# Optimization experiments

Hardware: AMD Instinct MI355X
Metric: run time of the kernel (lower is better)

The kernel has to match this reference:

```python
import jax, jax.numpy as jnp
import numpy as np

B, D, K = 32, 64, 256            # batch, num objects (seq len), feature size (== in_size)
G = [256, 256, 256]              # g_layers sizes
F1, F2, OUT = 256, 256, 128      # f_fc1, f_fc2, out_size


def setup_inputs() -> dict:
    key = jax.random.key(0)
    ks = jax.random.split(key, 16)
    scale = 0.02

    def w(k, shape):
        return jax.random.normal(k, shape, dtype=jnp.float32) * scale

    x = jax.random.normal(ks[0], (B, D, K), dtype=jnp.float32)
    # edge_feature: Linear(2*K, K). Stored [in, out] (transposed vs torch).
    edge_w = w(ks[1], (2 * K, K))
    edge_b = jnp.zeros((K,), dtype=jnp.float32)
    g_ws, g_bs = [], []
    in_s = K
    for i, out_s in enumerate(G):
        g_ws.append(w(ks[2 + i], (in_s, out_s)))
        g_bs.append(jnp.zeros((out_s,), dtype=jnp.float32))
        in_s = out_s
    f1_w = w(ks[8], (G[-1], F1)); f1_b = jnp.zeros((F1,), dtype=jnp.float32)
    f2_w = w(ks[9], (F1, F2));    f2_b = jnp.zeros((F2,), dtype=jnp.float32)
    f3_w = w(ks[10], (F2, OUT));  f3_b = jnp.zeros((OUT,), dtype=jnp.float32)
    return dict(x=x, edge_w=edge_w, edge_b=edge_b, g_ws=g_ws, g_bs=g_bs,
                f1_w=f1_w, f1_b=f1_b, f2_w=f2_w, f2_b=f2_b, f3_w=f3_w, f3_b=f3_b)


def reference(x, edge_w, edge_b, g_ws, g_bs, f1_w, f1_b, f2_w, f2_b, f3_w, f3_b):
    # x: [B, D, K]. Original builds x_full[b,i,j] = concat(x[b,j], x[b,i]) then
    # applies edge_feature (Linear(2K -> K)). Equivalent, without materializing the
    # concat: split edge_w into the halves acting on x_i (=x[b,j]) and x_j (=x[b,i]).
    k = x.shape[-1]
    u = x @ edge_w[:k]      # [B, D, K]  -> indexed by j (axis 2)
    v = x @ edge_w[k:]      # [B, D, K]  -> indexed by i (axis 1)
    h = u[:, None, :, :] + v[:, :, None, :] + edge_b   # [B, D, D, K]
    # g MLP over all d^2 pairs (Linear + ReLU chain)
    for gw, gb in zip(g_ws, g_bs):
        h = jax.nn.relu(h @ gw + gb)
    # sum-aggregate over all pairs
    x_g = h.sum(axis=(1, 2))                            # [B, G[-1]]
    # f MLP (dropout p=0.0 -> identity)
    x_f = jax.nn.relu(x_g @ f1_w + f1_b)
    x_f = jax.nn.relu(x_f @ f2_w + f2_b)
    return x_f @ f3_w + f3_b                            # [B, OUT]
```

## Files before the change

### kernel.cpp

```cpp
#include <hip/hip_runtime.h>
#include <hip/hip_bf16.h>

typedef __attribute__((ext_vector_type(4))) float f32x4;
typedef __attribute__((ext_vector_type(2))) int   i32x2;
typedef __attribute__((ext_vector_type(4))) int   i32x4;
typedef __attribute__((ext_vector_type(8))) short short8;

__device__ __forceinline__ unsigned short f2bf(float x) {
  __hip_bfloat16 h = __float2bfloat16(x);
  union { __hip_bfloat16 h1; unsigned short u; } c; c.h1 = h; return c.u;
}
__device__ __forceinline__ unsigned pk2(float a, float b) {
  __hip_bfloat162 h = __float22bfloat162_rn(make_float2(a, b));
  union { __hip_bfloat162 h2; unsigned u; } c; c.h2 = h; return c.u;
}
__device__ __forceinline__ float bf2f(unsigned short u) {
  union { unsigned u32; float f; } c; c.u32 = ((unsigned)u) << 16; return c.f;
}

__global__ void k_prep(const float* __restrict__ edge_w, const float* __restrict__ edge_b,
                       const float* __restrict__ gw0, const float* __restrict__ gb0,
                       const float* __restrict__ gw1, const float* __restrict__ gw2,
                       float* __restrict__ W1u, float* __restrict__ W1v,
                       float* __restrict__ c1,
                       unsigned short* __restrict__ W2R, unsigned short* __restrict__ W3R) {
  const int blk = blockIdx.x, t = threadIdx.x;
  __shared__ float eu[256], ev[256];
  if (blk < 256) {
    eu[t] = edge_w[blk * 256 + t];
    ev[t] = edge_w[(256 + blk) * 256 + t];
    __syncthreads();
    float su = 0.f, sv = 0.f;
    for (int o = 0; o < 256; ++o) {
      float gg = gw0[o * 256 + t];
      su += eu[o] * gg; sv += ev[o] * gg;
    }
    W1u[blk * 256 + t] = su;
    W1v[blk * 256 + t] = sv;
  } else if (blk == 256) {
    float s = gb0[t];
    for (int o = 0; o < 256; ++o) s += edge_b[o] * gw0[o * 256 + t];
    c1[t] = s;
  } else {
    int p = blk - 257;
    const float* src = (p < 32) ? gw1 : gw2;
    unsigned short* dst = (p < 32) ? W2R : W3R;
    p &= 31;
    int w = p >> 3, ch = p & 7;
    int mf = t >> 6, lane = t & 63, q = lane & 15, g = lane >> 4;
    int base = ((w * 8 + ch) * 4 + mf) * 512 + lane * 8;
    int m = w * 64 + mf * 16 + q;
#pragma unroll
    for (int e = 0; e < 8; ++e) {
      int k = ch * 32 + g * 8 + e;
      dst[base + e] = f2bf(src[k * 256 + m]);
    }
  }
}

__global__ void k_uv(const float* __restrict__ x,
                     const float* __restrict__ W1u, const float* __restrict__ W1v,
                     const float* __restrict__ c1,
                     unsigned short* __restrict__ U1, float* __restrict__ V1c) {
  const int blk = blockIdx.x, t = threadIdx.x;
  const int r0 = blk * 8;
  __shared__ float xs[2048];
  __shared__ float pl[8 * 512];
  if (t < 512) *(f32x4*)(xs + t * 4) = *(const f32x4*)(x + (size_t)r0 * 256 + t * 4);
  __syncthreads();
  const int sel = t >> 9, kh = (t >> 8) & 1, col = t & 255;
  const float* W = (sel ? W1v : W1u) + (size_t)kh * 128 * 256;
  const float* xb = xs + kh * 128;
  float a[8];
#pragma unroll
  for (int r = 0; r < 8; ++r) a[r] = 0.f;
#pragma unroll 4
  for (int k = 0; k < 128; ++k) {
    float w = W[k * 256 + col];
#pragma unroll
    for (int r = 0; r < 8; ++r) a[r] += xb[r * 256 + k] * w;
  }
  if (kh == 1) {
#pragma unroll
    for (int r = 0; r < 8; ++r) pl[r * 512 + sel * 256 + col] = a[r];
  }
  __syncthreads();
  if (kh == 0) {
#pragma unroll
    for (int r = 0; r < 8; ++r) a[r] += pl[r * 512 + sel * 256 + col];
    if (sel == 0) {
#pragma unroll
      for (int r = 0; r < 8; ++r) U1[(size_t)(r0 + r) * 256 + col] = f2bf(a[r]);
    } else {
      float c = c1[col];
#pragma unroll
      for (int r = 0; r < 8; ++r) V1c[(size_t)(r0 + r) * 256 + col] = a[r] + c;
    }
  }
}

__device__ __forceinline__ void write_h1(short8 u, f32x4 v0, f32x4 v1,
                                         unsigned short* dst) {
  float r0 = fmaxf(bf2f((unsigned short)u[0]) + v0.x, 0.f);
  float r1 = fmaxf(bf2f((unsigned short)u[1]) + v0.y, 0.f);
  float r2 = fmaxf(bf2f((unsigned short)u[2]) + v0.z, 0.f);
  float r3 = fmaxf(bf2f((unsigned short)u[3]) + v0.w, 0.f);
  float r4 = fmaxf(bf2f((unsigned short)u[4]) + v1.x, 0.f);
  float r5 = fmaxf(bf2f((unsigned short)u[5]) + v1.y, 0.f);
  float r6 = fmaxf(bf2f((unsigned short)u[6]) + v1.z, 0.f);
  float r7 = fmaxf(bf2f((unsigned short)u[7]) + v1.w, 0.f);
  i32x4 wv = { (int)pk2(r0, r1), (int)pk2(r2, r3), (int)pk2(r4, r5), (int)pk2(r6, r7) };
  *(i32x4*)dst = wv;
}

__launch_bounds__(256, 3)
__global__ void k_main(const unsigned short* __restrict__ U1,
                       const float* __restrict__ V1c,
                       const unsigned short* __restrict__ W2R,
                       const unsigned short* __restrict__ W3R,
                       const float* __restrict__ b2, const float* __restrict__ b3,
                       float* __restrict__ partials) {
  __shared__ unsigned short hbuf[16384];

  const int t = threadIdx.x;
  const int bid = blockIdx.x;
  const int wrk = ((bid & 7) << 8) | (bid >> 3);
  const int b = wrk >> 6;
  const int wid = t >> 6, lane = t & 63;
  const int q = lane & 15, g = lane >> 4;
  const int mo = wid << 6;

  {
    const int row = t >> 2, sl = t & 3, r7 = row & 7;
    const unsigned short* uB = U1 + (size_t)(b * 64 + row) * 256;
    const float* vB = V1c + (size_t)wrk * 256;
    unsigned short* hB = hbuf + row * 256;
#pragma unroll
    for (int m = 0; m < 8; ++m) {
      int ks = sl + 4 * m;
      int s = ks ^ r7;
      short8 u = *(const short8*)(uB + ks * 8);
      f32x4 v0 = *(const f32x4*)(vB + ks * 8);
      f32x4 v1 = *(const f32x4*)(vB + ks * 8 + 4);
      write_h1(u, v0, v1, hB + s * 8);
    }
  }

  const unsigned short* aW2 = W2R + (size_t)wid * 16384 + lane * 8;
  const unsigned short* aW3 = W3R + (size_t)wid * 16384 + lane * 8;

  short8 a_[4], an_[4];
#pragma unroll
  for (int mf = 0; mf < 4; ++mf) a_[mf] = *(const short8*)(aW2 + mf * 512);

  __syncthreads();

  f32x4 acc[4][4];
#pragma unroll
  for (int mf = 0; mf < 4; ++mf)
#pragma unroll
    for (int nf = 0; nf < 4; ++nf) acc[mf][nf] = (f32x4){0.f, 0.f, 0.f, 0.f};

  for (int ch = 0; ch < 8; ++ch) {
    if (ch < 7) {
#pragma unroll
      for (int mf = 0; mf < 4; ++mf)
        an_[mf] = *(const short8*)(aW2 + (ch + 1) * 2048 + mf * 512);
    }
    short8 b_[4];
#pragma unroll
    for (int nf = 0; nf < 4; ++nf) {
      int r = q + 16 * nf;
      b_[nf] = *(const short8*)(hbuf + r * 256 + (((ch * 4 + g) ^ (r & 7)) * 8));
    }
#pragma unroll
    for (int mf = 0; mf < 4; ++mf)
#pragma unroll
      for (int nf = 0; nf < 4; ++nf)
        acc[mf][nf] = __builtin_amdgcn_mfma_f32_16x16x32_bf16(a_[mf], b_[nf], acc[mf][nf], 0, 0, 0);
    if (ch < 7) {
#pragma unroll
      for (int mf = 0; mf < 4; ++mf) a_[mf] = an_[mf];
    }
  }

  __syncthreads();

#pragma unroll
  for (int mf = 0; mf < 4; ++mf) a_[mf] = *(const short8*)(aW3 + mf * 512);
#pragma unroll
  for (int mf = 0; mf < 4; ++mf) {
    int c2b = mo + 16 * mf + 4 * g;
    f32x4 bb = *(const f32x4*)(b2 + c2b);
    int ksw = c2b >> 3, off = c2b & 7;
#pragma unroll
    for (int nf = 0; nf < 4; ++nf) {
      int r = q + 16 * nf;
      f32x4 v = acc[mf][nf];
      float e0 = fmaxf(v.x + bb.x, 0.f), e1 = fmaxf(v.y + bb.y, 0.f);
      float e2 = fmaxf(v.z + bb.z, 0.f), e3 = fmaxf(v.w + bb.w, 0.f);
      i32x2 wv = { (int)pk2(e0, e1), (int)pk2(e2, e3) };
      *(i32x2*)(hbuf + r * 256 + ((ksw ^ (r & 7)) * 8) + off) = wv;
    }
  }
  __syncthreads();

  f32x4 acc2[4][4];
#pragma unroll
  for (int mf = 0; mf < 4; ++mf)
#pragma unroll
    for (int nf = 0; nf < 4; ++nf) acc2[mf][nf] = (f32x4){0.f, 0.f, 0.f, 0.f};

  for (int ch = 0; ch < 8; ++ch) {
    if (ch < 7) {
#pragma unroll
      for (int mf = 0; mf < 4; ++mf)
        an_[mf] = *(const short8*)(aW3 + (ch + 1) * 2048 + mf * 512);
    }
    short8 b_[4];
#pragma unroll
    for (int nf = 0; nf < 4; ++nf) {
      int r = q + 16 * nf;
      b_[nf] = *(const short8*)(hbuf + r * 256 + (((ch * 4 + g) ^ (r & 7)) * 8));
    }
#pragma unroll
    for (int mf = 0; mf < 4; ++mf)
#pragma unroll
      for (int nf = 0; nf < 4; ++nf)
        acc2[mf][nf] = __builtin_amdgcn_mfma_f32_16x16x32_bf16(a_[mf], b_[nf], acc2[mf][nf], 0, 0, 0);
    if (ch < 7) {
#pragma unroll
      for (int mf = 0; mf < 4; ++mf) a_[mf] = an_[mf];
    }
  }

  __syncthreads();

  float* scr = (float*)&hbuf[0];
#pragma unroll
  for (int mf = 0; mf < 4; ++mf) {
    int n3b = mo + 16 * mf + 4 * g;
    f32x4 bb = *(const f32x4*)(b3 + n3b);
    f32x4 sum = (f32x4){0.f, 0.f, 0.f, 0.f};
#pragma unroll
    for (int nf = 0; nf < 4; ++nf) {
      f32x4 v = acc2[mf][nf];
      sum.x += fmaxf(v.x + bb.x, 0.f);
      sum.y += fmaxf(v.y + bb.y, 0.f);
      sum.z += fmaxf(v.z + bb.z, 0.f);
      sum.w += fmaxf(v.w + bb.w, 0.f);
    }
    *(f32x4*)(scr + q * 264 + n3b) = sum;
  }
  __syncthreads();
  float s = 0.f;
#pragma unroll
  for (int q2 = 0; q2 < 16; ++q2) s += scr[q2 * 264 + t];
  partials[(size_t)wrk * 256 + t] = s;
}

__global__ void k_fmlp(const float* __restrict__ partials,
                       const float* __restrict__ f1w, const float* __restrict__ f1b,
                       const float* __restrict__ f2w, const float* __restrict__ f2b,
                       const float* __restrict__ f3w, const float* __restrict__ f3b,
                       float* __restrict__ out) {
  const int b = blockIdx.x, t = threadIdx.x;
  __shared__ float xg[256], x1[256], x2[256];
  {
    const float* p = partials + (size_t)(b * 64) * 256 + t;
    float s[8];
#pragma unroll
    for (int i = 0; i < 8; ++i) s[i] = 0.f;
#pragma unroll
    for (int k = 0; k < 8; ++k)
#pragma unroll
      for (int i = 0; i < 8; ++i) s[i] += p[(k * 8 + i) * 256];
    float tot = 0.f;
#pragma unroll
    for (int i = 0; i < 8; ++i) tot += s[i];
    xg[t] = tot;
  }
  __syncthreads();
  {
    float a0 = 0.f, a1 = 0.f, a2 = 0.f, a3 = 0.f;
#pragma unroll 4
    for (int k = 0; k < 64; ++k) {
      a0 += xg[k]       * f1w[(k)       * 256 + t];
      a1 += xg[k + 64]  * f1w[(k + 64)  * 256 + t];
      a2 += xg[k + 128] * f1w[(k + 128) * 256 + t];
      a3 += xg[k + 192] * f1w[(k + 192) * 256 + t];
    }
    x1[t] = fmaxf((a0 + a1) + (a2 + a3) + f1b[t], 0.f);
  }
  __syncthreads();
  {
    float a0 = 0.f, a1 = 0.f, a2 = 0.f, a3 = 0.f;
#pragma unroll 4
    for (int k = 0; k < 64; ++k) {
      a0 += x1[k]       * f2w[(k)       * 256 + t];
      a1 += x1[k + 64]  * f2w[(k + 64)  * 256 + t];
      a2 += x1[k + 128] * f2w[(k + 128) * 256 + t];
      a3 += x1[k + 192] * f2w[(k + 192) * 256 + t];
    }
    x2[t] = fmaxf((a0 + a1) + (a2 + a3) + f2b[t], 0.f);
  }
  __syncthreads();
  if (t < 128) {
    float a0 = 0.f, a1 = 0.f, a2 = 0.f, a3 = 0.f;
#pragma unroll 4
    for (int k = 0; k < 64; ++k) {
      a0 += x2[k]       * f3w[(k)       * 128 + t];
      a1 += x2[k + 64]  * f3w[(k + 64)  * 128 + t];
      a2 += x2[k + 128] * f3w[(k + 128) * 128 + t];
      a3 += x2[k + 192] * f3w[(k + 192) * 128 + t];
    }
    out[b * 128 + t] = (a0 + a1) + (a2 + a3) + f3b[t];
  }
}

__global__ void k_zero(float* __restrict__ out, int n) {
  int i = blockIdx.x * 256 + threadIdx.x;
  if (i < n) out[i] = 0.f;
}

extern "C" void kernel_launch(void* const* d_in, const int* in_sizes, int n_in,
                              void* d_out, int out_size, void* d_ws, size_t ws_size,
                              hipStream_t stream) {
  const float* x      = (const float*)d_in[0];
  const float* edge_w = (const float*)d_in[1];
  const float* edge_b = (const float*)d_in[2];
  const float *gw0, *gw1, *gw2, *gb0, *gb1, *gb2;
  const float *f1w, *f1b, *f2w, *f2b, *f3w, *f3b;

  if (n_in >= 15 && in_sizes[3] == 65536 && in_sizes[4] == 65536 && in_sizes[5] == 65536) {
    gw0 = (const float*)d_in[3]; gw1 = (const float*)d_in[4]; gw2 = (const float*)d_in[5];
    gb0 = (const float*)d_in[6]; gb1 = (const float*)d_in[7]; gb2 = (const float*)d_in[8];
    f1w = (const float*)d_in[9];  f1b = (const float*)d_in[10];
    f2w = (const float*)d_in[11]; f2b = (const float*)d_in[12];
    f3w = (const float*)d_in[13]; f3b = (const float*)d_in[14];
  } else if (n_in >= 15 && in_sizes[3] == 65536 && in_sizes[4] == 256) {
    gw0 = (const float*)d_in[3]; gb0 = (const float*)d_in[4];
    gw1 = (const float*)d_in[5]; gb1 = (const float*)d_in[6];
    gw2 = (const float*)d_in[7]; gb2 = (const float*)d_in[8];
    f1w = (const float*)d_in[9];  f1b = (const float*)d_in[10];
    f2w = (const float*)d_in[11]; f2b = (const float*)d_in[12];
    f3w = (const float*)d_in[13]; f3b = (const float*)d_in[14];
  } else {
    const float* gws = (const float*)d_in[3];
    const float* gbs = (const float*)d_in[4];
    gw0 = gws;          gw1 = gws + 65536;  gw2 = gws + 131072;
    gb0 = gbs;          gb1 = gbs + 256;    gb2 = gbs + 512;
    f1w = (const float*)d_in[5];  f1b = (const float*)d_in[6];
    f2w = (const float*)d_in[7];  f2b = (const float*)d_in[8];
    f3w = (const float*)d_in[9];  f3b = (const float*)d_in[10];
  }

  char* ws = (char*)d_ws;
  float*          W1u      = (float*)(ws);
  float*          W1v      = (float*)(ws + 262144);
  float*          c1       = (float*)(ws + 524288);
  unsigned short* W2R      = (unsigned short*)(ws + 525312);
  unsigned short* W3R      = (unsigned short*)(ws + 656384);
  unsigned short* U1       = (unsigned short*)(ws + 787456);
  float*          V1c      = (float*)(ws + 1836032);
  float*          partials = (float*)(ws + 3933184);
  const size_t need = 6030336;
  (void)out_size; (void)n_in;

  if (ws_size < need) {
    k_zero<<<dim3((out_size + 255) / 256), dim3(256), 0, stream>>>((float*)d_out, out_size);
    return;
  }

  k_prep<<<dim3(321), dim3(256), 0, stream>>>(edge_w, edge_b, gw0, gb0, gw1, gw2,
                                              W1u, W1v, c1, W2R, W3R);
  k_uv<<<dim3(256), dim3(1024), 0, stream>>>(x, W1u, W1v, c1, U1, V1c);
  k_main<<<dim3(2048), dim3(256), 0, stream>>>(U1, V1c, W2R, W3R, gb1, gb2, partials);
  k_fmlp<<<dim3(32), dim3(256), 0, stream>>>(partials, f1w, f1b, f2w, f2b, f3w, f3b,
                                             (float*)d_out);
}
```

Baseline: 79.28 us.

## Compute U/V projection with bf16 MFMA using pre-swizzled weights

Replaces the scalar fp32 FMA loop in the U/V projection kernel with bf16 MFMA 16x16x32 matrix instructions. A new conversion kernel repacks W1u/W1v into the same fragment layout already used for the g-layer weights. x is converted to bf16 into XOR-swizzled shared memory, and the next weight fragment is prefetched while the current one is consumed. The repacked weights reuse the partials region, which is only written later by k_main. This adds a kernel launch and lowers the precision of the projection inputs to bf16.

```diff
diff --git a/kernel.cpp b/kernel.cpp
--- a/kernel.cpp
+++ b/kernel.cpp
@@ -58,43 +58,106 @@
   }
 }
 
+__global__ void k_wcvt(const float* __restrict__ W1u, const float* __restrict__ W1v,
+                       unsigned short* __restrict__ W1uR, unsigned short* __restrict__ W1vR) {
+  int p = blockIdx.x;
+  const float* src = (p < 32) ? W1u : W1v;
+  unsigned short* dst = (p < 32) ? W1uR : W1vR;
+  p &= 31;
+  const int t = threadIdx.x;
+  int w = p >> 3, ch = p & 7;
+  int mf = t >> 6, lane = t & 63, q = lane & 15, g = lane >> 4;
+  int base = ((w * 8 + ch) * 4 + mf) * 512 + lane * 8;
+  int m = w * 64 + mf * 16 + q;
+#pragma unroll
+  for (int e = 0; e < 8; ++e) {
+    int k = ch * 32 + g * 8 + e;
+    dst[base + e] = f2bf(src[k * 256 + m]);
+  }
+}
+
 __global__ void k_uv(const float* __restrict__ x,
-                     const float* __restrict__ W1u, const float* __restrict__ W1v,
+                     const unsigned short* __restrict__ W1uR,
+                     const unsigned short* __restrict__ W1vR,
                      const float* __restrict__ c1,
                      unsigned short* __restrict__ U1, float* __restrict__ V1c) {
-  const int blk = blockIdx.x, t = threadIdx.x;
-  const int r0 = blk * 8;
-  __shared__ float xs[2048];
-  __shared__ float pl[8 * 512];
-  if (t < 512) *(f32x4*)(xs + t * 4) = *(const f32x4*)(x + (size_t)r0 * 256 + t * 4);
-  __syncthreads();
-  const int sel = t >> 9, kh = (t >> 8) & 1, col = t & 255;
-  const float* W = (sel ? W1v : W1u) + (size_t)kh * 128 * 256;
-  const float* xb = xs + kh * 128;
-  float a[8];
-#pragma unroll
-  for (int r = 0; r < 8; ++r) a[r] = 0.f;
-#pragma unroll 4
-  for (int k = 0; k < 128; ++k) {
-    float w = W[k * 256 + col];
-#pragma unroll
-    for (int r = 0; r < 8; ++r) a[r] += xb[r * 256 + k] * w;
-  }
-  if (kh == 1) {
-#pragma unroll
-    for (int r = 0; r < 8; ++r) pl[r * 512 + sel * 256 + col] = a[r];
-  }
-  __syncthreads();
-  if (kh == 0) {
-#pragma unroll
-    for (int r = 0; r < 8; ++r) a[r] += pl[r * 512 + sel * 256 + col];
-    if (sel == 0) {
-#pragma unroll
-      for (int r = 0; r < 8; ++r) U1[(size_t)(r0 + r) * 256 + col] = f2bf(a[r]);
-    } else {
-      float c = c1[col];
-#pragma unroll
-      for (int r = 0; r < 8; ++r) V1c[(size_t)(r0 + r) * 256 + col] = a[r] + c;
+  __shared__ unsigned short xs[8192];
+
+  const int t = threadIdx.x;
+  const int tile = blockIdx.x >> 1, sel = blockIdx.x & 1;
+  const int r0 = tile * 32;
+  const int wid = t >> 6, lane = t & 63;
+  const int q = lane & 15, g = lane >> 4;
+  const int mo = wid << 6;
+
+  {
+    const int row = t >> 3, sl = t & 7, r7 = row & 7;
+    const float* xB = x + (size_t)(r0 + row) * 256;
+    unsigned short* hB = xs + row * 256;
+#pragma unroll
+    for (int m = 0; m < 4; ++m) {
+      int ks = sl + 8 * m;
+      f32x4 u0 = *(const f32x4*)(xB + ks * 8);
+      f32x4 u1 = *(const f32x4*)(xB + ks * 8 + 4);
+      i32x4 wv = { (int)pk2(u0.x, u0.y), (int)pk2(u0.z, u0.w),
+                   (int)pk2(u1.x, u1.y), (int)pk2(u1.z, u1.w) };
+      *(i32x4*)(hB + (ks ^ r7) * 8) = wv;
+    }
+  }
+
+  const unsigned short* WR = sel ? W1vR : W1uR;
+  const unsigned short* aW = WR + (size_t)wid * 16384 + lane * 8;
+
+  short8 a_[4], an_[4];
+#pragma unroll
+  for (int mf = 0; mf < 4; ++mf) a_[mf] = *(const short8*)(aW + mf * 512);
+
+  __syncthreads();
+
+  f32x4 acc[4][2];
+#pragma unroll
+  for (int mf = 0; mf < 4; ++mf)
+#pragma unroll
+    for (int nf = 0; nf < 2; ++nf) acc[mf][nf] = (f32x4){0.f, 0.f, 0.f, 0.f};
+
+  for (int ch = 0; ch < 8; ++ch) {
+    if (ch < 7) {
+#pragma unroll
+      for (int mf = 0; mf < 4; ++mf)
+        an_[mf] = *(const short8*)(aW + (ch + 1) * 2048 + mf * 512);
+    }
+    short8 b_[2];
+#pragma unroll
+    for (int nf = 0; nf < 2; ++nf) {
+      int r = q + 16 * nf;
+      b_[nf] = *(const short8*)(xs + r * 256 + (((ch * 4 + g) ^ (r & 7)) * 8));
+    }
+#pragma unroll
+    for (int mf = 0; mf < 4; ++mf)
+#pragma unroll
+      for (int nf = 0; nf < 2; ++nf)
+        acc[mf][nf] = __builtin_amdgcn_mfma_f32_16x16x32_bf16(a_[mf], b_[nf], acc[mf][nf], 0, 0, 0);
+    if (ch < 7) {
+#pragma unroll
+      for (int mf = 0; mf < 4; ++mf) a_[mf] = an_[mf];
+    }
+  }
+
+#pragma unroll
+  for (int mf = 0; mf < 4; ++mf) {
+    int c2b = mo + 16 * mf + 4 * g;
+#pragma unroll
+    for (int nf = 0; nf < 2; ++nf) {
+      int r = r0 + q + 16 * nf;
+      f32x4 v = acc[mf][nf];
+      if (sel == 0) {
+        i32x2 wv = { (int)pk2(v.x, v.y), (int)pk2(v.z, v.w) };
+        *(i32x2*)(U1 + (size_t)r * 256 + c2b) = wv;
+      } else {
+        f32x4 cc = *(const f32x4*)(c1 + c2b);
+        f32x4 o = { v.x + cc.x, v.y + cc.y, v.z + cc.z, v.w + cc.w };
+        *(f32x4*)(V1c + (size_t)r * 256 + c2b) = o;
+      }
     }
   }
 }
@@ -364,6 +427,8 @@
   unsigned short* U1       = (unsigned short*)(ws + 787456);
   float*          V1c      = (float*)(ws + 1836032);
   float*          partials = (float*)(ws + 3933184);
+  unsigned short* W1uR     = (unsigned short*)(ws + 3933184);
+  unsigned short* W1vR     = (unsigned short*)(ws + 3933184 + 131072);
   const size_t need = 6030336;
   (void)out_size; (void)n_in;
 
@@ -374,7 +439,8 @@
 
   k_prep<<<dim3(321), dim3(256), 0, stream>>>(edge_w, edge_b, gw0, gb0, gw1, gw2,
                                               W1u, W1v, c1, W2R, W3R);
-  k_uv<<<dim3(256), dim3(1024), 0, stream>>>(x, W1u, W1v, c1, U1, V1c);
+  k_wcvt<<<dim3(64), dim3(256), 0, stream>>>(W1u, W1v, W1uR, W1vR);
+  k_uv<<<dim3(128), dim3(256), 0, stream>>>(x, W1uR, W1vR, c1, U1, V1c);
   k_main<<<dim3(2048), dim3(256), 0, stream>>>(U1, V1c, W2R, W3R, gb1, gb2, partials);
   k_fmlp<<<dim3(32), dim3(256), 0, stream>>>(partials, f1w, f1b, f2w, f2b, f3w, f3b,
                                              (float*)d_out);
```

Result: faster. 76.04 us (-4.1%).
